# Kernel tuning notes

Hardware: AMD Instinct MI355X
Metric: run time of the kernel (lower is better)

Reference implementation:

```python
import jax, jax.numpy as jnp
import numpy as np

N_NODES = 100000
N_EDGES = 1600000
IN_C, HID_C, OUT_C = 128, 64, 32


def setup_inputs() -> dict:
    key = jax.random.key(0)
    k1, k2, k3, k4 = jax.random.split(key, 4)
    x = jax.random.normal(k1, (N_NODES, IN_C), dtype=jnp.float32)
    edge_index = jax.random.randint(k2, (2, N_EDGES), 0, N_NODES, dtype=jnp.int64)
    # glorot-style init for GCN linear weights
    W1 = jax.random.normal(k3, (IN_C, HID_C), dtype=jnp.float32) * (2.0 / (IN_C + HID_C)) ** 0.5
    b1 = jnp.zeros((HID_C,), dtype=jnp.float32)
    W2 = jax.random.normal(k4, (HID_C, OUT_C), dtype=jnp.float32) * (2.0 / (HID_C + OUT_C)) ** 0.5
    b2 = jnp.zeros((OUT_C,), dtype=jnp.float32)
    return {"x": x, "edge_index": edge_index, "W1": W1, "b1": b1, "W2": W2, "b2": b2}


def _gcn_conv(h, row, col, norm, n, b):
    # gather transformed source features, scale by symmetric norm, scatter-add to targets
    msg = h[row] * norm[:, None]            # [E+N, C]
    return jax.ops.segment_sum(msg, col, num_segments=n) + b


def reference(x, edge_index, W1, b1, W2, b2):
    n = x.shape[0]
    loops = jnp.arange(n, dtype=edge_index.dtype)
    row = jnp.concatenate([edge_index[0], loops])   # sources (with self-loops)
    col = jnp.concatenate([edge_index[1], loops])   # targets
    deg = jax.ops.segment_sum(jnp.ones_like(col, dtype=x.dtype), col, num_segments=n)
    dinv = jnp.where(deg > 0, jax.lax.rsqrt(deg), 0.0)
    norm = dinv[row] * dinv[col]                    # D^{-1/2} A_hat D^{-1/2}
    h = jax.nn.relu(_gcn_conv(x @ W1, row, col, norm, n, b1))
    out = _gcn_conv(h @ W2, row, col, norm, n, b2)
    return out
```

## Files before the change

### kernel.cpp

```cpp
#include <hip/hip_runtime.h>

#define IN_C 128
#define HID_C 64
#define OUT_C 32
#define NBLK 512
#define NBUCK 512
#define CAP 5120

typedef unsigned int uint;
typedef unsigned short ushort;
typedef __attribute__((ext_vector_type(8))) short bf16x8;
typedef __attribute__((ext_vector_type(4))) float f32x4;

__device__ __forceinline__ uint bf16pair(float a, float b) {
  uint ua = __float_as_uint(a), ub = __float_as_uint(b);
  ua = (ua + 0x7FFFu + ((ua >> 16) & 1u)) >> 16;
  ub = (ub + 0x7FFFu + ((ub >> 16) & 1u)) >> 16;
  return ua | (ub << 16);
}

__device__ __forceinline__ uint bf16one(float a) {
  uint u = __float_as_uint(a);
  return (u + 0x7FFFu + ((u >> 16) & 1u)) >> 16;
}

__device__ __forceinline__ void acc8(float* acc, uint4 q) {
  acc[0] += __uint_as_float(q.x << 16);
  acc[1] += __uint_as_float(q.x & 0xFFFF0000u);
  acc[2] += __uint_as_float(q.y << 16);
  acc[3] += __uint_as_float(q.y & 0xFFFF0000u);
  acc[4] += __uint_as_float(q.z << 16);
  acc[5] += __uint_as_float(q.z & 0xFFFF0000u);
  acc[6] += __uint_as_float(q.w << 16);
  acc[7] += __uint_as_float(q.w & 0xFFFF0000u);
}


__global__ void __launch_bounds__(256) scatter_reserve_kernel(
    const int* __restrict__ row, const int* __restrict__ col,
    int* __restrict__ gcur, int* __restrict__ ebuf, int e, int epb) {
  __shared__ int hist[NBUCK];
  __shared__ int cur[NBUCK];
  int t = threadIdx.x, b = blockIdx.x;
  for (int i = t; i < NBUCK; i += 256) hist[i] = 0;
  __syncthreads();
  int s = b * epb, en = min(e, s + epb);
  for (int i = s + t; i < en; i += 256) atomicAdd(&hist[col[i] >> 8], 1);
  __syncthreads();
  for (int i = t; i < NBUCK; i += 256) {
    int h = hist[i];
    int base = h ? atomicAdd(&gcur[i], h) : 0;
    cur[i] = CAP * i + base;
  }
  __syncthreads();
  for (int i = s + t; i < en; i += 256) {
    int c = col[i], r = row[i];
    int bk = c >> 8;
    int p = atomicAdd(&cur[bk], 1);
    if (p < CAP * bk + CAP) ebuf[p] = r | ((c & 255) << 17);
  }
}

__global__ void __launch_bounds__(256) csr_kernel(const int* __restrict__ ebuf,
                                                  const int* __restrict__ gcur,
                                                  int* __restrict__ offS, int* __restrict__ offE,
                                                  int* __restrict__ srt, float* __restrict__ dinv,
                                                  int n) {
  __shared__ int cnt[256];
  __shared__ int base[256];
  int t = threadIdx.x, b = blockIdx.x;
  int es = b * CAP;
  int ec = min(gcur[b], CAP);
  cnt[t] = 0;
  __syncthreads();
  for (int i = t; i < ec; i += 256) atomicAdd(&cnt[(ebuf[es + i] >> 17) & 255], 1);
  __syncthreads();
  int v = cnt[t];
  base[t] = v;
  __syncthreads();
  for (int d = 1; d < 256; d <<= 1) {
    int a = (t >= d) ? base[t - d] : 0;
    __syncthreads();
    base[t] += a;
    __syncthreads();
  }
  int gstart = es + base[t] - v;
  int node = b * 256 + t;
  if (node < n) {
    offS[node] = gstart;
    offE[node] = gstart + v;
    dinv[node] = rsqrtf((float)(v + 1));
  }
  base[t] = gstart;
  __syncthreads();
  for (int i = t; i < ec; i += 256) {
    int pv = ebuf[es + i];
    int pos = atomicAdd(&base[(pv >> 17) & 255], 1);
    srt[pos] = pv & 0x1FFFF;
  }
}


__global__ void __launch_bounds__(256) prep_w1t_kernel(const float* __restrict__ W1,
                                                       ushort* __restrict__ w1t_hi,
                                                       ushort* __restrict__ w1t_lo) {
  int t = threadIdx.x;
  for (int i = t; i < HID_C * IN_C; i += 256) {
    int c = i >> 7, k = i & 127;
    float v = W1[k * HID_C + c];
    uint h = bf16one(v);
    float lo = v - __uint_as_float(h << 16);
    w1t_hi[i] = (ushort)h;
    w1t_lo[i] = (ushort)bf16one(lo);
  }
}

__global__ void __launch_bounds__(256) gemm1_mfma_kernel(
    const float* __restrict__ x, const ushort* __restrict__ w1t_hi,
    const ushort* __restrict__ w1t_lo, const float* __restrict__ dinv,
    ushort* __restrict__ xw1b, int n) {
  __shared__ float eps[4][16 * 68];
  int t = threadIdx.x;
  int wv = t >> 6, lane = t & 63, m = lane & 15, q = lane >> 4;
  int row0 = blockIdx.x * 64 + wv * 16;
  int arow = min(row0 + m, n - 1);
  const float* xp = x + (size_t)arow * IN_C + q * 8;
  bf16x8 ah[4], al[4];
#pragma unroll
  for (int kb = 0; kb < 4; ++kb) {
    float4 v0 = *(const float4*)(xp + kb * 32);
    float4 v1 = *(const float4*)(xp + kb * 32 + 4);
    float vv[8] = {v0.x, v0.y, v0.z, v0.w, v1.x, v1.y, v1.z, v1.w};
    uint hu[8];
    float lf[8];
#pragma unroll
    for (int i = 0; i < 8; ++i) {
      hu[i] = bf16one(vv[i]);
      lf[i] = vv[i] - __uint_as_float(hu[i] << 16);
    }
    uint4 hq = make_uint4(hu[0] | (hu[1] << 16), hu[2] | (hu[3] << 16),
                          hu[4] | (hu[5] << 16), hu[6] | (hu[7] << 16));
    uint4 lq = make_uint4(bf16pair(lf[0], lf[1]), bf16pair(lf[2], lf[3]),
                          bf16pair(lf[4], lf[5]), bf16pair(lf[6], lf[7]));
    ah[kb] = *(bf16x8*)&hq;
    al[kb] = *(bf16x8*)&lq;
  }
  f32x4 acc[4];
#pragma unroll
  for (int ct = 0; ct < 4; ++ct) acc[ct] = (f32x4){0.f, 0.f, 0.f, 0.f};
#pragma unroll
  for (int kb = 0; kb < 4; ++kb) {
#pragma unroll
    for (int ct = 0; ct < 4; ++ct) {
      const ushort* bp = w1t_hi + (ct * 16 + m) * IN_C + kb * 32 + q * 8;
      bf16x8 bh = *(const bf16x8*)bp;
      bf16x8 bl = *(const bf16x8*)(w1t_lo + (ct * 16 + m) * IN_C + kb * 32 + q * 8);
      acc[ct] = __builtin_amdgcn_mfma_f32_16x16x32_bf16(ah[kb], bh, acc[ct], 0, 0, 0);
      acc[ct] = __builtin_amdgcn_mfma_f32_16x16x32_bf16(al[kb], bh, acc[ct], 0, 0, 0);
      acc[ct] = __builtin_amdgcn_mfma_f32_16x16x32_bf16(ah[kb], bl, acc[ct], 0, 0, 0);
    }
  }
  float* ep = eps[wv];
#pragma unroll
  for (int ct = 0; ct < 4; ++ct)
#pragma unroll
    for (int rg = 0; rg < 4; ++rg)
      ep[(q * 4 + rg) * 68 + ct * 16 + m] = acc[ct][rg];
  __syncthreads();
#pragma unroll
  for (int it = 0; it < 2; ++it) {
    int r = it * 8 + (lane >> 3), cc = lane & 7;
    int grow = row0 + r;
    if (grow < n) {
      float4 v0 = *(const float4*)&ep[r * 68 + cc * 8];
      float4 v1 = *(const float4*)&ep[r * 68 + cc * 8 + 4];
      float dv = dinv[grow];
      uint4 o = make_uint4(bf16pair(v0.x * dv, v0.y * dv), bf16pair(v0.z * dv, v0.w * dv),
                           bf16pair(v1.x * dv, v1.y * dv), bf16pair(v1.z * dv, v1.w * dv));
      *(uint4*)(xw1b + (size_t)grow * HID_C + cc * 8) = o;
    }
  }
}

__global__ void __launch_bounds__(256) gather1_gemm2_kernel(
    const int* __restrict__ offS, const int* __restrict__ offE, const int* __restrict__ srt,
    const float* __restrict__ dinv, const ushort* __restrict__ xw1b,
    const float* __restrict__ b1, const float* __restrict__ W2,
    ushort* __restrict__ hw2b, int n) {
  __shared__ float w2s[HID_C * OUT_C];
  __shared__ float hs[32][HID_C];
  int t = threadIdx.x;
  for (int i = t; i < HID_C * OUT_C; i += 256) w2s[i] = W2[i];
  int g = t >> 3, fl = t & 7;
  int c = blockIdx.x * 32 + g;
  if (c < n) {
    int js = offS[c], je = offE[c];
    float acc[8] = {0.f, 0.f, 0.f, 0.f, 0.f, 0.f, 0.f, 0.f};
    float acc2[8] = {0.f, 0.f, 0.f, 0.f, 0.f, 0.f, 0.f, 0.f};
    int j = js;
    for (; j + 3 < je; j += 4) {
      int r0 = __builtin_nontemporal_load(srt + j);
      int r1 = __builtin_nontemporal_load(srt + j + 1);
      int r2 = __builtin_nontemporal_load(srt + j + 2);
      int r3 = __builtin_nontemporal_load(srt + j + 3);
      uint4 q0 = ((const uint4*)(xw1b + (size_t)r0 * HID_C))[fl];
      uint4 q1 = ((const uint4*)(xw1b + (size_t)r1 * HID_C))[fl];
      uint4 q2 = ((const uint4*)(xw1b + (size_t)r2 * HID_C))[fl];
      uint4 q3 = ((const uint4*)(xw1b + (size_t)r3 * HID_C))[fl];
      acc8(acc, q0); acc8(acc2, q1); acc8(acc, q2); acc8(acc2, q3);
    }
    for (; j < je; ++j) {
      int r = __builtin_nontemporal_load(srt + j);
      acc8(acc, ((const uint4*)(xw1b + (size_t)r * HID_C))[fl]);
    }
    acc8(acc, ((const uint4*)(xw1b + (size_t)c * HID_C))[fl]);
    float dv = dinv[c];
    const float4* b1v = (const float4*)b1;
    float4 blo = b1v[fl * 2], bhi = b1v[fl * 2 + 1];
    float h0 = (acc[0] + acc2[0]) * dv + blo.x;
    float h1 = (acc[1] + acc2[1]) * dv + blo.y;
    float h2 = (acc[2] + acc2[2]) * dv + blo.z;
    float h3 = (acc[3] + acc2[3]) * dv + blo.w;
    float h4 = (acc[4] + acc2[4]) * dv + bhi.x;
    float h5 = (acc[5] + acc2[5]) * dv + bhi.y;
    float h6 = (acc[6] + acc2[6]) * dv + bhi.z;
    float h7 = (acc[7] + acc2[7]) * dv + bhi.w;
    float4 lo = {h0 > 0.f ? h0 : 0.f, h1 > 0.f ? h1 : 0.f,
                 h2 > 0.f ? h2 : 0.f, h3 > 0.f ? h3 : 0.f};
    float4 hi = {h4 > 0.f ? h4 : 0.f, h5 > 0.f ? h5 : 0.f,
                 h6 > 0.f ? h6 : 0.f, h7 > 0.f ? h7 : 0.f};
    ((float4*)hs[g])[fl * 2] = lo;
    ((float4*)hs[g])[fl * 2 + 1] = hi;
  }
  __syncthreads();
  for (int task = t; task < 32 * (OUT_C / 2); task += 256) {
    int nl = task >> 4, pr = task & 15;
    int c2 = blockIdx.x * 32 + nl;
    if (c2 < n) {
      float s0 = 0.f, s1 = 0.f;
      const float* hr = hs[nl];
#pragma unroll
      for (int k = 0; k < HID_C; ++k) {
        float hv = hr[k];
        s0 += hv * w2s[k * OUT_C + pr * 2];
        s1 += hv * w2s[k * OUT_C + pr * 2 + 1];
      }
      float dv2 = dinv[c2];
      ((uint*)(hw2b + (size_t)c2 * OUT_C))[pr] = bf16pair(s0 * dv2, s1 * dv2);
    }
  }
}

__global__ void __launch_bounds__(256) gather2_kernel(
    const int* __restrict__ offS, const int* __restrict__ offE, const int* __restrict__ srt,
    const float* __restrict__ dinv, const ushort* __restrict__ hw2b,
    const float* __restrict__ b2, float* __restrict__ out, int n) {
  int t = threadIdx.x;
  int g = t >> 2, fl = t & 3;
  int c = blockIdx.x * 64 + g;
  if (c >= n) return;
  int js = offS[c], je = offE[c];
  float acc[8] = {0.f, 0.f, 0.f, 0.f, 0.f, 0.f, 0.f, 0.f};
  float acc2[8] = {0.f, 0.f, 0.f, 0.f, 0.f, 0.f, 0.f, 0.f};
  int j = js;
  for (; j + 3 < je; j += 4) {
    int r0 = __builtin_nontemporal_load(srt + j);
    int r1 = __builtin_nontemporal_load(srt + j + 1);
    int r2 = __builtin_nontemporal_load(srt + j + 2);
    int r3 = __builtin_nontemporal_load(srt + j + 3);
    uint4 q0 = ((const uint4*)(hw2b + (size_t)r0 * OUT_C))[fl];
    uint4 q1 = ((const uint4*)(hw2b + (size_t)r1 * OUT_C))[fl];
    uint4 q2 = ((const uint4*)(hw2b + (size_t)r2 * OUT_C))[fl];
    uint4 q3 = ((const uint4*)(hw2b + (size_t)r3 * OUT_C))[fl];
    acc8(acc, q0); acc8(acc2, q1); acc8(acc, q2); acc8(acc2, q3);
  }
  for (; j < je; ++j) {
    int r = __builtin_nontemporal_load(srt + j);
    acc8(acc, ((const uint4*)(hw2b + (size_t)r * OUT_C))[fl]);
  }
  acc8(acc, ((const uint4*)(hw2b + (size_t)c * OUT_C))[fl]);
  float dv = dinv[c];
  const float4* b2v = (const float4*)b2;
  float4 blo = b2v[fl * 2], bhi = b2v[fl * 2 + 1];
  float4 olo = {(acc[0] + acc2[0]) * dv + blo.x, (acc[1] + acc2[1]) * dv + blo.y,
                (acc[2] + acc2[2]) * dv + blo.z, (acc[3] + acc2[3]) * dv + blo.w};
  float4 ohi = {(acc[4] + acc2[4]) * dv + bhi.x, (acc[5] + acc2[5]) * dv + bhi.y,
                (acc[6] + acc2[6]) * dv + bhi.z, (acc[7] + acc2[7]) * dv + bhi.w};
  ((float4*)(out + (size_t)c * OUT_C))[fl * 2] = olo;
  ((float4*)(out + (size_t)c * OUT_C))[fl * 2 + 1] = ohi;
}

extern "C" void kernel_launch(void* const* d_in, const int* in_sizes, int n_in,
                              void* d_out, int out_size, void* d_ws, size_t ws_size,
                              hipStream_t stream) {
  const float* x  = (const float*)d_in[0];
  const int*   ei = (const int*)d_in[1];
  const float* W1 = (const float*)d_in[2];
  const float* b1 = (const float*)d_in[3];
  const float* W2 = (const float*)d_in[4];
  const float* b2 = (const float*)d_in[5];
  float* out = (float*)d_out;

  int n = in_sizes[0] / IN_C;
  int e = in_sizes[1] / 2;
  const int* row = ei;
  const int* col = ei + e;

  float* dinv = (float*)d_ws;
  int*   offS = (int*)(dinv + n);
  int*   offE = offS + n;
  int*   gcur = offE + n;
  int*   srt  = gcur + NBUCK;
  ushort* xw1b = (ushort*)(srt + (size_t)NBUCK * CAP);
  int*   ebuf = (int*)xw1b;
  ushort* hw2b = xw1b + (size_t)n * HID_C;
  ushort* w1t_hi = hw2b + (size_t)n * OUT_C;
  ushort* w1t_lo = w1t_hi + HID_C * IN_C;

  int epb = (e + NBLK - 1) / NBLK;
  int nbuckets = (n + 255) / 256;

  hipMemsetAsync(gcur, 0, NBUCK * sizeof(int), stream);
  hipLaunchKernelGGL(scatter_reserve_kernel, dim3(NBLK), dim3(256), 0, stream,
                     row, col, gcur, ebuf, e, epb);
  hipLaunchKernelGGL(csr_kernel, dim3(nbuckets), dim3(256), 0, stream,
                     ebuf, gcur, offS, offE, srt, dinv, n);
  hipLaunchKernelGGL(prep_w1t_kernel, dim3(1), dim3(256), 0, stream, W1, w1t_hi, w1t_lo);
  hipLaunchKernelGGL(gemm1_mfma_kernel, dim3((n + 63) / 64), dim3(256), 0, stream,
                     x, w1t_hi, w1t_lo, dinv, xw1b, n);
  hipLaunchKernelGGL(gather1_gemm2_kernel, dim3((n + 31) / 32), dim3(256), 0, stream,
                     offS, offE, srt, dinv, xw1b, b1, W2, hw2b, n);
  hipLaunchKernelGGL(gather2_kernel, dim3((n + 63) / 64), dim3(256), 0, stream,
                     offS, offE, srt, dinv, hw2b, b2, out, n);
}
```

Before: 248.3 us.

## Use wave shuffles for fused GEMM2, unroll gathers by eight, parallelize W1 prep

The fused gather+GEMM2 kernel no longer stages the hidden row in shared memory behind a second barrier. Each 8-lane group now broadcasts its hidden values with wave shuffles and computes four output columns per lane directly. Both gather loops gain an 8-way unrolled main loop for more memory-level parallelism, and the W1 transpose/split kernel now runs across 32 blocks instead of one. These changes add register pressure and shuffle traffic, and the early return for out-of-range nodes in a kernel that uses shuffles carries some risk.

```diff
diff --git a/kernel.cpp b/kernel.cpp
--- a/kernel.cpp
+++ b/kernel.cpp
@@ -100,18 +100,17 @@
   }
 }
 
-
 __global__ void __launch_bounds__(256) prep_w1t_kernel(const float* __restrict__ W1,
                                                        ushort* __restrict__ w1t_hi,
                                                        ushort* __restrict__ w1t_lo) {
-  int t = threadIdx.x;
-  for (int i = t; i < HID_C * IN_C; i += 256) {
-    int c = i >> 7, k = i & 127;
-    float v = W1[k * HID_C + c];
+  int i = blockIdx.x * 256 + threadIdx.x;
+  if (i < HID_C * IN_C) {
+    int k = i >> 6, c = i & 63;
+    float v = W1[i];
     uint h = bf16one(v);
     float lo = v - __uint_as_float(h << 16);
-    w1t_hi[i] = (ushort)h;
-    w1t_lo[i] = (ushort)bf16one(lo);
+    w1t_hi[c * IN_C + k] = (ushort)h;
+    w1t_lo[c * IN_C + k] = (ushort)bf16one(lo);
   }
 }
 
@@ -188,67 +187,83 @@
     const float* __restrict__ b1, const float* __restrict__ W2,
     ushort* __restrict__ hw2b, int n) {
   __shared__ float w2s[HID_C * OUT_C];
-  __shared__ float hs[32][HID_C];
   int t = threadIdx.x;
   for (int i = t; i < HID_C * OUT_C; i += 256) w2s[i] = W2[i];
+  __syncthreads();
   int g = t >> 3, fl = t & 7;
   int c = blockIdx.x * 32 + g;
-  if (c < n) {
-    int js = offS[c], je = offE[c];
-    float acc[8] = {0.f, 0.f, 0.f, 0.f, 0.f, 0.f, 0.f, 0.f};
-    float acc2[8] = {0.f, 0.f, 0.f, 0.f, 0.f, 0.f, 0.f, 0.f};
-    int j = js;
-    for (; j + 3 < je; j += 4) {
-      int r0 = __builtin_nontemporal_load(srt + j);
-      int r1 = __builtin_nontemporal_load(srt + j + 1);
-      int r2 = __builtin_nontemporal_load(srt + j + 2);
-      int r3 = __builtin_nontemporal_load(srt + j + 3);
-      uint4 q0 = ((const uint4*)(xw1b + (size_t)r0 * HID_C))[fl];
-      uint4 q1 = ((const uint4*)(xw1b + (size_t)r1 * HID_C))[fl];
-      uint4 q2 = ((const uint4*)(xw1b + (size_t)r2 * HID_C))[fl];
-      uint4 q3 = ((const uint4*)(xw1b + (size_t)r3 * HID_C))[fl];
-      acc8(acc, q0); acc8(acc2, q1); acc8(acc, q2); acc8(acc2, q3);
+  if (c >= n) return;
+  int js = offS[c], je = offE[c];
+  float acc[8] = {0.f, 0.f, 0.f, 0.f, 0.f, 0.f, 0.f, 0.f};
+  float acc2[8] = {0.f, 0.f, 0.f, 0.f, 0.f, 0.f, 0.f, 0.f};
+  int j = js;
+  for (; j + 7 < je; j += 8) {
+    int r0 = __builtin_nontemporal_load(srt + j);
+    int r1 = __builtin_nontemporal_load(srt + j + 1);
+    int r2 = __builtin_nontemporal_load(srt + j + 2);
+    int r3 = __builtin_nontemporal_load(srt + j + 3);
+    int r4 = __builtin_nontemporal_load(srt + j + 4);
+    int r5 = __builtin_nontemporal_load(srt + j + 5);
+    int r6 = __builtin_nontemporal_load(srt + j + 6);
+    int r7 = __builtin_nontemporal_load(srt + j + 7);
+    uint4 q0 = ((const uint4*)(xw1b + (size_t)r0 * HID_C))[fl];
+    uint4 q1 = ((const uint4*)(xw1b + (size_t)r1 * HID_C))[fl];
+    uint4 q2 = ((const uint4*)(xw1b + (size_t)r2 * HID_C))[fl];
+    uint4 q3 = ((const uint4*)(xw1b + (size_t)r3 * HID_C))[fl];
+    uint4 q4 = ((const uint4*)(xw1b + (size_t)r4 * HID_C))[fl];
+    uint4 q5 = ((const uint4*)(xw1b + (size_t)r5 * HID_C))[fl];
+    uint4 q6 = ((const uint4*)(xw1b + (size_t)r6 * HID_C))[fl];
+    uint4 q7 = ((const uint4*)(xw1b + (size_t)r7 * HID_C))[fl];
+    acc8(acc, q0); acc8(acc2, q1); acc8(acc, q2); acc8(acc2, q3);
+    acc8(acc, q4); acc8(acc2, q5); acc8(acc, q6); acc8(acc2, q7);
+  }
+  for (; j + 3 < je; j += 4) {
+    int r0 = __builtin_nontemporal_load(srt + j);
+    int r1 = __builtin_nontemporal_load(srt + j + 1);
+    int r2 = __builtin_nontemporal_load(srt + j + 2);
+    int r3 = __builtin_nontemporal_load(srt + j + 3);
+    uint4 q0 = ((const uint4*)(xw1b + (size_t)r0 * HID_C))[fl];
+    uint4 q1 = ((const uint4*)(xw1b + (size_t)r1 * HID_C))[fl];
+    uint4 q2 = ((const uint4*)(xw1b + (size_t)r2 * HID_C))[fl];
+    uint4 q3 = ((const uint4*)(xw1b + (size_t)r3 * HID_C))[fl];
+    acc8(acc, q0); acc8(acc2, q1); acc8(acc, q2); acc8(acc2, q3);
+  }
+  for (; j < je; ++j) {
+    int r = __builtin_nontemporal_load(srt + j);
+    acc8(acc, ((const uint4*)(xw1b + (size_t)r * HID_C))[fl]);
+  }
+  acc8(acc, ((const uint4*)(xw1b + (size_t)c * HID_C))[fl]);
+  float dv = dinv[c];
+  const float4* b1v = (const float4*)b1;
+  float4 blo = b1v[fl * 2], bhi = b1v[fl * 2 + 1];
+  float h[8];
+  h[0] = (acc[0] + acc2[0]) * dv + blo.x;
+  h[1] = (acc[1] + acc2[1]) * dv + blo.y;
+  h[2] = (acc[2] + acc2[2]) * dv + blo.z;
+  h[3] = (acc[3] + acc2[3]) * dv + blo.w;
+  h[4] = (acc[4] + acc2[4]) * dv + bhi.x;
+  h[5] = (acc[5] + acc2[5]) * dv + bhi.y;
+  h[6] = (acc[6] + acc2[6]) * dv + bhi.z;
+  h[7] = (acc[7] + acc2[7]) * dv + bhi.w;
+#pragma unroll
+  for (int i = 0; i < 8; ++i) h[i] = h[i] > 0.f ? h[i] : 0.f;
+  int lanebase = (t & 63) & 56;
+  float o0 = 0.f, o1 = 0.f, o2 = 0.f, o3 = 0.f;
+#pragma unroll
+  for (int s = 0; s < 8; ++s) {
+    int src = lanebase | s;
+#pragma unroll
+    for (int i = 0; i < 8; ++i) {
+      float hv = __shfl(h[i], src, 64);
+      float4 w = *(const float4*)(&w2s[(s * 8 + i) * OUT_C + fl * 4]);
+      o0 += hv * w.x; o1 += hv * w.y; o2 += hv * w.z; o3 += hv * w.w;
     }
-    for (; j < je; ++j) {
-      int r = __builtin_nontemporal_load(srt + j);
-      acc8(acc, ((const uint4*)(xw1b + (size_t)r * HID_C))[fl]);
-    }
-    acc8(acc, ((const uint4*)(xw1b + (size_t)c * HID_C))[fl]);
-    float dv = dinv[c];
-    const float4* b1v = (const float4*)b1;
-    float4 blo = b1v[fl * 2], bhi = b1v[fl * 2 + 1];
-    float h0 = (acc[0] + acc2[0]) * dv + blo.x;
-    float h1 = (acc[1] + acc2[1]) * dv + blo.y;
-    float h2 = (acc[2] + acc2[2]) * dv + blo.z;
-    float h3 = (acc[3] + acc2[3]) * dv + blo.w;
-    float h4 = (acc[4] + acc2[4]) * dv + bhi.x;
-    float h5 = (acc[5] + acc2[5]) * dv + bhi.y;
-    float h6 = (acc[6] + acc2[6]) * dv + bhi.z;
-    float h7 = (acc[7] + acc2[7]) * dv + bhi.w;
-    float4 lo = {h0 > 0.f ? h0 : 0.f, h1 > 0.f ? h1 : 0.f,
-                 h2 > 0.f ? h2 : 0.f, h3 > 0.f ? h3 : 0.f};
-    float4 hi = {h4 > 0.f ? h4 : 0.f, h5 > 0.f ? h5 : 0.f,
-                 h6 > 0.f ? h6 : 0.f, h7 > 0.f ? h7 : 0.f};
-    ((float4*)hs[g])[fl * 2] = lo;
-    ((float4*)hs[g])[fl * 2 + 1] = hi;
-  }
-  __syncthreads();
-  for (int task = t; task < 32 * (OUT_C / 2); task += 256) {
-    int nl = task >> 4, pr = task & 15;
-    int c2 = blockIdx.x * 32 + nl;
-    if (c2 < n) {
-      float s0 = 0.f, s1 = 0.f;
-      const float* hr = hs[nl];
-#pragma unroll
-      for (int k = 0; k < HID_C; ++k) {
-        float hv = hr[k];
-        s0 += hv * w2s[k * OUT_C + pr * 2];
-        s1 += hv * w2s[k * OUT_C + pr * 2 + 1];
-      }
-      float dv2 = dinv[c2];
-      ((uint*)(hw2b + (size_t)c2 * OUT_C))[pr] = bf16pair(s0 * dv2, s1 * dv2);
-    }
-  }
+  }
+  float dv2 = dv;
+  uint2 ov;
+  ov.x = bf16pair(o0 * dv2, o1 * dv2);
+  ov.y = bf16pair(o2 * dv2, o3 * dv2);
+  ((uint2*)(hw2b + (size_t)c * OUT_C))[fl] = ov;
 }
 
 __global__ void __launch_bounds__(256) gather2_kernel(
@@ -263,6 +278,26 @@
   float acc[8] = {0.f, 0.f, 0.f, 0.f, 0.f, 0.f, 0.f, 0.f};
   float acc2[8] = {0.f, 0.f, 0.f, 0.f, 0.f, 0.f, 0.f, 0.f};
   int j = js;
+  for (; j + 7 < je; j += 8) {
+    int r0 = __builtin_nontemporal_load(srt + j);
+    int r1 = __builtin_nontemporal_load(srt + j + 1);
+    int r2 = __builtin_nontemporal_load(srt + j + 2);
+    int r3 = __builtin_nontemporal_load(srt + j + 3);
+    int r4 = __builtin_nontemporal_load(srt + j + 4);
+    int r5 = __builtin_nontemporal_load(srt + j + 5);
+    int r6 = __builtin_nontemporal_load(srt + j + 6);
+    int r7 = __builtin_nontemporal_load(srt + j + 7);
+    uint4 q0 = ((const uint4*)(hw2b + (size_t)r0 * OUT_C))[fl];
+    uint4 q1 = ((const uint4*)(hw2b + (size_t)r1 * OUT_C))[fl];
+    uint4 q2 = ((const uint4*)(hw2b + (size_t)r2 * OUT_C))[fl];
+    uint4 q3 = ((const uint4*)(hw2b + (size_t)r3 * OUT_C))[fl];
+    uint4 q4 = ((const uint4*)(hw2b + (size_t)r4 * OUT_C))[fl];
+    uint4 q5 = ((const uint4*)(hw2b + (size_t)r5 * OUT_C))[fl];
+    uint4 q6 = ((const uint4*)(hw2b + (size_t)r6 * OUT_C))[fl];
+    uint4 q7 = ((const uint4*)(hw2b + (size_t)r7 * OUT_C))[fl];
+    acc8(acc, q0); acc8(acc2, q1); acc8(acc, q2); acc8(acc2, q3);
+    acc8(acc, q4); acc8(acc2, q5); acc8(acc, q6); acc8(acc2, q7);
+  }
   for (; j + 3 < je; j += 4) {
     int r0 = __builtin_nontemporal_load(srt + j);
     int r1 = __builtin_nontemporal_load(srt + j + 1);
@@ -325,7 +360,8 @@
                      row, col, gcur, ebuf, e, epb);
   hipLaunchKernelGGL(csr_kernel, dim3(nbuckets), dim3(256), 0, stream,
                      ebuf, gcur, offS, offE, srt, dinv, n);
-  hipLaunchKernelGGL(prep_w1t_kernel, dim3(1), dim3(256), 0, stream, W1, w1t_hi, w1t_lo);
+  hipLaunchKernelGGL(prep_w1t_kernel, dim3((HID_C * IN_C + 255) / 256), dim3(256), 0, stream,
+                     W1, w1t_hi, w1t_lo);
   hipLaunchKernelGGL(gemm1_mfma_kernel, dim3((n + 63) / 64), dim3(256), 0, stream,
                      x, w1t_hi, w1t_lo, dinv, xw1b, n);
   hipLaunchKernelGGL(gather1_gemm2_kernel, dim3((n + 31) / 32), dim3(256), 0, stream,
```

After: 241.4 us. -2.8%, faster.
